# Kernel tuning notes

Hardware: AMD Instinct MI355X
Metric: run time of the kernel (lower is better)

## Reference

```python
import jax, jax.numpy as jnp
import numpy as np

NL = 8      # num layers (['self','cross']*4)
H = 8       # heads
EPS = 1e-5  # torch LayerNorm default


def _layernorm(x, g, b):
    mu = jnp.mean(x, axis=-1, keepdims=True)
    var = jnp.mean((x - mu) ** 2, axis=-1, keepdims=True)
    return (x - mu) * jax.lax.rsqrt(var + EPS) * g + b


def _encoder_layer(x, source, Wq, Wk, Wv, Wm, W1, W2, g1, b1, g2, b2):
    # x: [N, L, C], source: [N, S, C]
    N, L, C = x.shape
    D = C // H
    q = (x @ Wq).reshape(N, L, H, D)
    k = (source @ Wk).reshape(N, -1, H, D)
    v = (source @ Wv).reshape(N, -1, H, D)
    # naive full attention: explicit [N, L, S, H] scores (as in FullAttention)
    qk = jnp.einsum('nlhd,nshd->nlsh', q, k)
    A = jax.nn.softmax(qk * (1.0 / np.sqrt(D)), axis=2)
    msg = jnp.einsum('nlsh,nshd->nlhd', A, v).reshape(N, L, C)
    msg = _layernorm(msg @ Wm, g1, b1)
    m = jnp.concatenate([x, msg], axis=-1)          # [N, L, 2C]
    m = jax.nn.relu(m @ W1) @ W2                    # [N, L, C]
    m = _layernorm(m, g2, b2)
    return x + m


def _loftr(feat0, feat1, Wq, Wk, Wv, Wm, W1, W2, g1, b1, g2, b2):
    names = ['self', 'cross'] * 4
    for i, name in enumerate(names):
        p = (Wq[i], Wk[i], Wv[i], Wm[i], W1[i], W2[i], g1[i], b1[i], g2[i], b2[i])
        if name == 'self':
            feat0 = _encoder_layer(feat0, feat0, *p)
            feat1 = _encoder_layer(feat1, feat1, *p)
        else:  # cross; note feat0 is updated before being fed to feat1's layer
            feat0 = _encoder_layer(feat0, feat1, *p)
            feat1 = _encoder_layer(feat1, feat0, *p)
    return jnp.stack([feat0, feat1], axis=0)  # [2, N, L, C]


def setup_inputs() -> dict:
    key = jax.random.key(0)
    ks = jax.random.split(key, 10)
    N, L, C = 8, 1024, 768
    s = 1.0 / np.sqrt(C)       # xavier-ish scale for [C, C]
    s2 = 1.0 / np.sqrt(2 * C)  # for MLP fan-in 2C
    return {
        'feat0': jax.random.normal(ks[0], (N, L, C), jnp.float32),
        'feat1': jax.random.normal(ks[1], (N, L, C), jnp.float32),
        'Wq': jax.random.normal(ks[2], (NL, C, C), jnp.float32) * s,
        'Wk': jax.random.normal(ks[3], (NL, C, C), jnp.float32) * s,
        'Wv': jax.random.normal(ks[4], (NL, C, C), jnp.float32) * s,
        'Wm': jax.random.normal(ks[5], (NL, C, C), jnp.float32) * s,
        'W1': jax.random.normal(ks[6], (NL, 2 * C, 2 * C), jnp.float32) * s2,
        'W2': jax.random.normal(ks[7], (NL, 2 * C, C), jnp.float32) * s2,
        'g1': jnp.ones((NL, C), jnp.float32),
        'b1': jnp.zeros((NL, C), jnp.float32),
        'g2': jnp.ones((NL, C), jnp.float32),
        'b2': jnp.zeros((NL, C), jnp.float32),
    }


def reference(feat0, feat1, Wq, Wk, Wv, Wm, W1, W2, g1, b1, g2, b2):
    return _loftr(feat0, feat1, Wq, Wk, Wv, Wm, W1, W2, g1, b1, g2, b2)
```

## Files before the change

kernel.cpp:

```cpp
#include <hip/hip_runtime.h>
#include <hip/hip_bf16.h>

typedef __hip_bfloat16 bf16;
typedef __bf16 bf16x8 __attribute__((ext_vector_type(8)));
typedef float f32x4 __attribute__((ext_vector_type(4)));

#define AS1 __attribute__((address_space(1)))
#define AS3 __attribute__((address_space(3)))
__device__ __forceinline__ void gl_lds16(const void* g, void* l) {
    __builtin_amdgcn_global_load_lds((const AS1 void*)g, (AS3 void*)l, 16, 0, 0);
}

__device__ __forceinline__ float fexp2(float x) {
#if __has_builtin(__builtin_amdgcn_exp2f)
    return __builtin_amdgcn_exp2f(x);
#else
    return exp2f(x);
#endif
}

__device__ __forceinline__ int xcd_swz(int did, int nwg) {
    return (did & 7) * (nwg >> 3) + (did >> 3);
}


__global__ __launch_bounds__(256) void cvt_f32_bf16_k(const float* __restrict__ in, bf16* __restrict__ out,
                                                      int ostride, int total)
{
    int i = blockIdx.x * 256 + threadIdx.x;
    int e = i * 4;
    if (e >= total) return;
    int row = e / 768;
    int col = e - row * 768;
    const float4 f = *(const float4*)(in + e);
    bf16 o4[4];
    o4[0] = __float2bfloat16(f.x); o4[1] = __float2bfloat16(f.y);
    o4[2] = __float2bfloat16(f.z); o4[3] = __float2bfloat16(f.w);
    *(uint2*)(out + (size_t)row * ostride + col) = *(uint2*)o4;
}

__global__ void transpose_cvt_k(const float* __restrict__ in, bf16* __restrict__ out, int R, int C,
                                float scale, size_t lstride)
{
    __shared__ float t[32][33];
    const int tx = threadIdx.x, ty = threadIdx.y;
    in  += (size_t)blockIdx.z * R * C;
    out += (size_t)blockIdx.z * lstride;
    const int c0 = blockIdx.x * 32, r0 = blockIdx.y * 32;
    #pragma unroll
    for (int i = 0; i < 4; ++i)
        t[ty + i*8][tx] = in[(size_t)(r0 + ty + i*8) * C + c0 + tx];
    __syncthreads();
    #pragma unroll
    for (int i = 0; i < 4; ++i)
        out[(size_t)(c0 + ty + i*8) * R + r0 + tx] = __float2bfloat16(t[tx][ty + i*8] * scale);
}

template<int EPI>
__global__ __launch_bounds__(256) void gemm_bt_k(const bf16* __restrict__ A, int lda,
                                                 const bf16* __restrict__ BT, int K,
                                                 void* __restrict__ Cp, int ldc, int colshift,
                                                 bf16* __restrict__ Ck, bf16* __restrict__ Cv)
{
    __shared__ bf16 a_sm[3][4096];
    __shared__ bf16 b_sm[3][4096];
    const int tid = threadIdx.x;
    const int lane = tid & 63;
    const int wid = tid >> 6;
    const int wr = wid >> 1, wc = wid & 1;

    const int nwg = gridDim.x * gridDim.y;
    const int did = blockIdx.x + gridDim.x * blockIdx.y;
    const int wgid = xcd_swz(did, nwg);
    const int col0 = (wgid % gridDim.y) * 128;
    const int row0 = (wgid / gridDim.y) * 128;
    const int g = lane >> 4, r16 = lane & 15;

    const int r4 = lane >> 2;
    const int sc = (lane & 3) ^ ((lane >> 3) & 3);
    const bf16* gA[2]; const bf16* gB[2]; int loff[2];
    #pragma unroll
    for (int i = 0; i < 2; ++i) {
        const int blk = wid*2 + i;
        gA[i] = A  + (size_t)(row0 + blk*16 + r4) * lda + sc*8;
        gB[i] = BT + (size_t)(col0 + blk*16 + r4) * K   + sc*8;
        loff[i] = blk * 512;
    }
    const int foff = r16*32 + ((g ^ ((r16 >> 1) & 3)) * 8);

    f32x4 acc[4][4];
    #pragma unroll
    for (int m = 0; m < 4; ++m)
        #pragma unroll
        for (int n = 0; n < 4; ++n)
            #pragma unroll
            for (int r = 0; r < 4; ++r) acc[m][n][r] = 0.f;

    #pragma unroll
    for (int i = 0; i < 2; ++i) {
        gl_lds16(gA[i],      &a_sm[0][loff[i]]);
        gl_lds16(gB[i],      &b_sm[0][loff[i]]);
    }
    #pragma unroll
    for (int i = 0; i < 2; ++i) {
        gl_lds16(gA[i] + 32, &a_sm[1][loff[i]]);
        gl_lds16(gB[i] + 32, &b_sm[1][loff[i]]);
    }

    int cur = 0, pre = 2;
    for (int k0 = 0; k0 < K; k0 += 32) {
        if (k0 + 32 < K) asm volatile("s_waitcnt vmcnt(4)" ::: "memory");
        else             asm volatile("s_waitcnt vmcnt(0)" ::: "memory");
        __builtin_amdgcn_s_barrier();
        if (k0 + 64 < K) {
            #pragma unroll
            for (int i = 0; i < 2; ++i) {
                gl_lds16(gA[i] + k0 + 64, &a_sm[pre][loff[i]]);
                gl_lds16(gB[i] + k0 + 64, &b_sm[pre][loff[i]]);
            }
        }
        bf16x8 af[4], bfr[4];
        #pragma unroll
        for (int m = 0; m < 4; ++m) af[m]  = *(const bf16x8*)&a_sm[cur][(wr*4 + m)*512 + foff];
        #pragma unroll
        for (int n = 0; n < 4; ++n) bfr[n] = *(const bf16x8*)&b_sm[cur][(wc*4 + n)*512 + foff];
        asm volatile("s_waitcnt lgkmcnt(0)" ::: "memory");
        __builtin_amdgcn_s_setprio(1);
        #pragma unroll
        for (int m = 0; m < 4; ++m)
            #pragma unroll
            for (int n = 0; n < 4; ++n)
                acc[m][n] = __builtin_amdgcn_mfma_f32_16x16x32_bf16(af[m], bfr[n], acc[m][n], 0, 0, 0);
        __builtin_amdgcn_s_setprio(0);
        cur = (cur == 2) ? 0 : cur + 1;
        pre = (pre == 2) ? 0 : pre + 1;
    }

    #pragma unroll
    for (int m = 0; m < 4; ++m) {
        const int orow = row0 + wr*64 + m*16 + g*4;
        #pragma unroll
        for (int n = 0; n < 4; ++n) {
            const int ocol = col0 + wc*64 + n*16 + r16;
            if (EPI == 4 || EPI == 5) {
                const int ce = ocol + colshift;
                const int seg = ce / 768;
                const int ci = ce - seg*768;
                if (seg <= 1) {
                    bf16* dst = (seg == 0) ? (bf16*)Cp : Ck;
                    #pragma unroll
                    for (int r = 0; r < 4; ++r)
                        dst[(size_t)(orow + r)*768 + ci] = __float2bfloat16(acc[m][n][r]);
                } else {
                    const int nn = orow >> 10, ss = orow & 1023;
                    const int hh = ci / 96, dd = ci - hh * 96;
                    bf16 pk[4];
                    #pragma unroll
                    for (int r = 0; r < 4; ++r) pk[r] = __float2bfloat16(acc[m][n][r]);
                    *(uint2*)&Cv[(((size_t)nn*8 + hh)*96 + dd)*1024 + ss] = *(uint2*)pk;
                }
            } else {
                #pragma unroll
                for (int r = 0; r < 4; ++r) {
                    float v = acc[m][n][r];
                    if (EPI == 1) v = fmaxf(v, 0.f);
                    ((bf16*)Cp)[(size_t)(orow + r)*ldc + ocol] = __float2bfloat16(v);
                }
            }
        }
    }
}

__global__ __launch_bounds__(512) void attn_k(const bf16* __restrict__ qb, const bf16* __restrict__ kb,
                                              const bf16* __restrict__ vtb, bf16* __restrict__ msgb)
{
    __shared__ bf16 kv_sm[3][12*512];
    __shared__ bf16 p_sm_all[8][32][40];
    const int tid = threadIdx.x;
    const int lane = tid & 63;
    const int w = tid >> 6;
    const int g = lane >> 4, r16 = lane & 15;

    const int nwg = gridDim.x * gridDim.y;
    const int did = blockIdx.x + gridDim.x * blockIdx.y;
    const int wgid = xcd_swz(did, nwg);
    const int qx = wgid % gridDim.x;
    const int nh = wgid / gridDim.x;
    const int n = nh >> 3, h = nh & 7;
    const int q0 = qx * 256 + w * 32;

    bf16 (*p_sm)[40] = p_sm_all[w];

    const bf16* kbase = kb  + ((size_t)n*1024)*768 + (size_t)h*96;
    const bf16* vbase = vtb + ((size_t)(n*8 + h))*96*1024;

    bf16x8 aq[2][3];
    #pragma unroll
    for (int qh = 0; qh < 2; ++qh) {
        const size_t qoff = ((size_t)n*1024 + q0 + qh*16 + r16) * 768 + (size_t)h*96;
        #pragma unroll
        for (int c = 0; c < 3; ++c) aq[qh][c] = *(const bf16x8*)&qb[qoff + c*32 + g*8];
    }

    const int r4 = lane >> 2;
    const int sc = (lane & 3) ^ ((lane >> 3) & 3);
    const bf16* gsrc[2]; size_t gstep[2]; int dstoff[2];
    const int nissue = (w < 4) ? 2 : 1;
    #pragma unroll
    for (int jj = 0; jj < 2; ++jj) {
        const int issue = w + jj*8;
        if (issue < 6) {
            const int c = issue >> 1, kh = issue & 1;
            gsrc[jj]  = kbase + (size_t)(kh*16 + r4)*768 + c*32 + sc*8;
            gstep[jj] = 768;
        } else {
            gsrc[jj]  = vbase + (size_t)((issue-6)*16 + r4)*1024 + sc*8;
            gstep[jj] = 1;
        }
        dstoff[jj] = (issue < 12) ? issue * 512 : 0;
    }
    const int foff = r16*32 + ((g ^ ((r16 >> 1) & 3)) * 8);

    float m_run[2], l_run[2];
    #pragma unroll
    for (int qh = 0; qh < 2; ++qh) { m_run[qh] = -1e30f; l_run[qh] = 0.f; }
    f32x4 o[2][6];
    #pragma unroll
    for (int qg = 0; qg < 2; ++qg)
        #pragma unroll
        for (int f = 0; f < 6; ++f)
            #pragma unroll
            for (int r = 0; r < 4; ++r) o[qg][f][r] = 0.f;

    gl_lds16(gsrc[0], &kv_sm[0][dstoff[0]]);
    if (nissue == 2) gl_lds16(gsrc[1], &kv_sm[0][dstoff[1]]);
    gl_lds16(gsrc[0] + 32 * gstep[0], &kv_sm[1][dstoff[0]]);
    if (nissue == 2) gl_lds16(gsrc[1] + 32 * gstep[1], &kv_sm[1][dstoff[1]]);

    int cur = 0, pre = 2;
    for (int kt = 0; kt < 1024; kt += 32) {
        if (kt + 32 < 1024) {
            if (nissue == 2) asm volatile("s_waitcnt vmcnt(2)" ::: "memory");
            else             asm volatile("s_waitcnt vmcnt(1)" ::: "memory");
        } else {
            asm volatile("s_waitcnt vmcnt(0)" ::: "memory");
        }
        __builtin_amdgcn_s_barrier();
        if (kt + 64 < 1024) {
            gl_lds16(gsrc[0] + (size_t)(kt + 64) * gstep[0], &kv_sm[pre][dstoff[0]]);
            if (nissue == 2) gl_lds16(gsrc[1] + (size_t)(kt + 64) * gstep[1], &kv_sm[pre][dstoff[1]]);
        }
        const bf16* rd = kv_sm[cur];

        f32x4 s[2][2];
        #pragma unroll
        for (int kh = 0; kh < 2; ++kh)
            #pragma unroll
            for (int qh = 0; qh < 2; ++qh)
                #pragma unroll
                for (int r = 0; r < 4; ++r) s[kh][qh][r] = 0.f;
        __builtin_amdgcn_s_setprio(1);
        #pragma unroll
        for (int c = 0; c < 3; ++c) {
            bf16x8 ak0 = *(const bf16x8*)&rd[(c*2 + 0)*512 + foff];
            bf16x8 ak1 = *(const bf16x8*)&rd[(c*2 + 1)*512 + foff];
            s[0][0] = __builtin_amdgcn_mfma_f32_16x16x32_bf16(ak0, aq[0][c], s[0][0], 0, 0, 0);
            s[0][1] = __builtin_amdgcn_mfma_f32_16x16x32_bf16(ak0, aq[1][c], s[0][1], 0, 0, 0);
            s[1][0] = __builtin_amdgcn_mfma_f32_16x16x32_bf16(ak1, aq[0][c], s[1][0], 0, 0, 0);
            s[1][1] = __builtin_amdgcn_mfma_f32_16x16x32_bf16(ak1, aq[1][c], s[1][1], 0, 0, 0);
        }
        __builtin_amdgcn_s_setprio(0);

        float pmv[2], gr[2];
        #pragma unroll
        for (int qh = 0; qh < 2; ++qh) {
            float pm = fmaxf(fmaxf(fmaxf(s[0][qh][0], s[0][qh][1]), fmaxf(s[0][qh][2], s[0][qh][3])),
                             fmaxf(fmaxf(s[1][qh][0], s[1][qh][1]), fmaxf(s[1][qh][2], s[1][qh][3])));
            pm = fmaxf(pm, __shfl_xor(pm, 16, 64));
            pm = fmaxf(pm, __shfl_xor(pm, 32, 64));
            pmv[qh] = pm;
            gr[qh] = pm - m_run[qh];
        }
        if (__any(fmaxf(gr[0], gr[1]) > 8.0f)) {
            float alpha_c[2];
            #pragma unroll
            for (int qh = 0; qh < 2; ++qh) {
                float mn = fmaxf(m_run[qh], pmv[qh]);
                alpha_c[qh] = fexp2(m_run[qh] - mn);
                m_run[qh] = mn;
                l_run[qh] *= alpha_c[qh];
            }
            #pragma unroll
            for (int qg = 0; qg < 2; ++qg)
                #pragma unroll
                for (int r = 0; r < 4; ++r) {
                    float ar = __shfl(alpha_c[qg], g*4 + r, 64);
                    #pragma unroll
                    for (int f = 0; f < 6; ++f) o[qg][f][r] *= ar;
                }
        }
        #pragma unroll
        for (int qh = 0; qh < 2; ++qh) {
            bf16 pk0[4], pk1[4];
            float rs = 0.f;
            #pragma unroll
            for (int r = 0; r < 4; ++r) {
                float p0 = fexp2(s[0][qh][r] - m_run[qh]);
                float p1 = fexp2(s[1][qh][r] - m_run[qh]);
                rs += p0 + p1;
                pk0[r] = __float2bfloat16(p0);
                pk1[r] = __float2bfloat16(p1);
            }
            rs += __shfl_xor(rs, 16, 64);
            rs += __shfl_xor(rs, 32, 64);
            l_run[qh] += rs;
            *(uint2*)&p_sm[qh*16 + r16][g*4]      = *(uint2*)pk0;
            *(uint2*)&p_sm[qh*16 + r16][16 + g*4] = *(uint2*)pk1;
        }

        bf16x8 pa0 = *(const bf16x8*)&p_sm[r16][g*8];
        bf16x8 pa1 = *(const bf16x8*)&p_sm[16 + r16][g*8];
        __builtin_amdgcn_s_setprio(1);
        #pragma unroll
        for (int f = 0; f < 6; ++f) {
            bf16x8 bv = *(const bf16x8*)&rd[(6 + f)*512 + foff];
            o[0][f] = __builtin_amdgcn_mfma_f32_16x16x32_bf16(pa0, bv, o[0][f], 0, 0, 0);
            o[1][f] = __builtin_amdgcn_mfma_f32_16x16x32_bf16(pa1, bv, o[1][f], 0, 0, 0);
        }
        __builtin_amdgcn_s_setprio(0);
        asm volatile("s_waitcnt lgkmcnt(0)" ::: "memory");
        cur = (cur == 2) ? 0 : cur + 1;
        pre = (pre == 2) ? 0 : pre + 1;
    }

    float linv[2][4];
    #pragma unroll
    for (int qg = 0; qg < 2; ++qg)
        #pragma unroll
        for (int r = 0; r < 4; ++r)
            linv[qg][r] = 1.0f / __shfl(l_run[qg], g*4 + r, 64);

    #pragma unroll
    for (int qg = 0; qg < 2; ++qg) {
        const size_t obase = ((size_t)n*1024 + q0 + qg*16 + g*4) * 768 + (size_t)h*96;
        #pragma unroll
        for (int f = 0; f < 6; ++f)
            #pragma unroll
            for (int r = 0; r < 4; ++r)
                msgb[obase + (size_t)r*768 + f*16 + r16] = __float2bfloat16(o[qg][f][r] * linv[qg][r]);
    }
}

template<int MODE>
__global__ __launch_bounds__(256) void ln_k(const bf16* __restrict__ in, const float* __restrict__ g,
                                            const float* __restrict__ b, bf16* __restrict__ outc,
                                            float* __restrict__ x)
{
    const int row = blockIdx.x;
    const int tid = threadIdx.x;
    const bf16* rp = in + (size_t)row * 768;
    float v[3];
    #pragma unroll
    for (int j = 0; j < 3; ++j) v[j] = __bfloat162float(rp[tid + j*256]);
    float s  = v[0] + v[1] + v[2];
    float sq = v[0]*v[0] + v[1]*v[1] + v[2]*v[2];
    #pragma unroll
    for (int off = 32; off >= 1; off >>= 1) {
        s  += __shfl_xor(s,  off, 64);
        sq += __shfl_xor(sq, off, 64);
    }
    __shared__ float red[2][4];
    const int wid = tid >> 6;
    if ((tid & 63) == 0) { red[0][wid] = s; red[1][wid] = sq; }
    __syncthreads();
    const float S  = red[0][0] + red[0][1] + red[0][2] + red[0][3];
    const float SQ = red[1][0] + red[1][1] + red[1][2] + red[1][3];
    const float mu = S * (1.f/768.f);
    float var = SQ * (1.f/768.f) - mu*mu;
    var = fmaxf(var, 0.f);
    const float rs = rsqrtf(var + 1e-5f);
    #pragma unroll
    for (int j = 0; j < 3; ++j) {
        const int c = tid + j*256;
        const float y = (v[j] - mu) * rs * g[c] + b[c];
        if (MODE == 1) {
            outc[(size_t)row*1536 + 768 + c] = __float2bfloat16(y);
        } else {
            const float nx = x[(size_t)row*768 + c] + y;
            x[(size_t)row*768 + c] = nx;
            outc[(size_t)row*1536 + c] = __float2bfloat16(nx);
        }
    }
}

extern "C" void kernel_launch(void* const* d_in, const int* in_sizes, int n_in,
                              void* d_out, int out_size, void* d_ws, size_t ws_size,
                              hipStream_t stream)
{
    const float* feat0 = (const float*)d_in[0];
    const float* feat1 = (const float*)d_in[1];
    const float* Wq = (const float*)d_in[2];
    const float* Wk = (const float*)d_in[3];
    const float* Wv = (const float*)d_in[4];
    const float* Wm = (const float*)d_in[5];
    const float* W1 = (const float*)d_in[6];
    const float* W2 = (const float*)d_in[7];
    const float* g1 = (const float*)d_in[8];
    const float* b1 = (const float*)d_in[9];
    const float* g2 = (const float*)d_in[10];
    const float* b2 = (const float*)d_in[11];

    bf16 *wqkvT, *wmT, *w1T, *w2T, *concat0, *concat1, *qb, *kb, *vtb, *m1b, *t0b;
    auto plan = [&](int RB) -> size_t {
        char* p = (char*)d_ws;
        auto take = [&](size_t bytes) { char* q = p; p += (bytes + 255) & ~(size_t)255; return q; };
        wqkvT = (bf16*)take((size_t)8*2304*768*2);
        wmT  = (bf16*)take((size_t)8*768*768*2);
        w1T  = (bf16*)take((size_t)8*1536*1536*2);
        w2T  = (bf16*)take((size_t)8*768*1536*2);
        concat0 = (bf16*)take((size_t)8192*1536*2);
        concat1 = (bf16*)take((size_t)8192*1536*2);
        qb   = (bf16*)take((size_t)RB*768*2);
        kb   = (bf16*)take((size_t)RB*768*2);
        vtb  = (bf16*)take((size_t)RB*768*2);
        m1b  = (bf16*)take((size_t)RB*1536*2);
        t0b  = (bf16*)take((size_t)RB*768*2);
        return (size_t)(p - (char*)d_ws);
    };
    bool batched = plan(16384) <= ws_size;
    if (!batched) plan(8192);
    bf16* msgb = qb;

    float* x0 = (float*)d_out;
    float* x1 = x0 + (size_t)8192*768;

    hipMemcpyAsync(x0, feat0, (size_t)8192*768*4, hipMemcpyDeviceToDevice, stream);
    hipMemcpyAsync(x1, feat1, (size_t)8192*768*4, hipMemcpyDeviceToDevice, stream);

    const float s_qk = 0.14724444f;
    const dim3 tb(32, 8);
    const size_t QKV = (size_t)2304*768;
    transpose_cvt_k<<<dim3(24,24,8), tb, 0, stream>>>(Wq, wqkvT,            768, 768,  s_qk, QKV);
    transpose_cvt_k<<<dim3(24,24,8), tb, 0, stream>>>(Wk, wqkvT + 768*768,  768, 768,  1.0f, QKV);
    transpose_cvt_k<<<dim3(24,24,8), tb, 0, stream>>>(Wv, wqkvT + 1536*768, 768, 768,  1.0f, QKV);
    transpose_cvt_k<<<dim3(24,24,8), tb, 0, stream>>>(Wm, wmT, 768, 768,  1.0f, (size_t)768*768);
    transpose_cvt_k<<<dim3(48,48,8), tb, 0, stream>>>(W1, w1T, 1536, 1536, 1.0f, (size_t)1536*1536);
    transpose_cvt_k<<<dim3(24,48,8), tb, 0, stream>>>(W2, w2T, 1536, 768,  1.0f, (size_t)1536*768);

    const int total = 8192*768;
    cvt_f32_bf16_k<<<6144, 256, 0, stream>>>(feat0, concat0, 1536, total);
    cvt_f32_bf16_k<<<6144, 256, 0, stream>>>(feat1, concat1, 1536, total);

    auto encode = [&](float* x, bf16* cS, const bf16* cR, int i, bool self, int M) {
        const bf16* wl = wqkvT + (size_t)i * QKV;
        const int MT = M / 128;
        if (self) {
            gemm_bt_k<4><<<dim3(MT,18), 256, 0, stream>>>(cS, 1536, wl, 768, qb, 768, 0, kb, vtb);
        } else {
            gemm_bt_k<0><<<dim3(MT,6),  256, 0, stream>>>(cS, 1536, wl, 768, qb, 768, 0, nullptr, nullptr);
            gemm_bt_k<5><<<dim3(MT,12), 256, 0, stream>>>(cR, 1536, wl + (size_t)768*768, 768,
                                                          nullptr, 0, 768, kb, vtb);
        }
        attn_k<<<dim3(4, (M/1024)*8), 512, 0, stream>>>(qb, kb, vtb, msgb);
        gemm_bt_k<0><<<dim3(MT,6),  256, 0, stream>>>(msgb, 768, wmT + (size_t)i*768*768, 768,
                                                      t0b, 768, 0, nullptr, nullptr);
        ln_k<1><<<M, 256, 0, stream>>>(t0b, g1 + i*768, b1 + i*768, cS, nullptr);
        gemm_bt_k<1><<<dim3(MT,12), 256, 0, stream>>>(cS, 1536, w1T + (size_t)i*1536*1536, 1536,
                                                      m1b, 1536, 0, nullptr, nullptr);
        gemm_bt_k<0><<<dim3(MT,6),  256, 0, stream>>>(m1b, 1536, w2T + (size_t)i*768*1536, 1536,
                                                      t0b, 768, 0, nullptr, nullptr);
        ln_k<2><<<M, 256, 0, stream>>>(t0b, g2 + i*768, b2 + i*768, cS, x);
    };

    for (int i = 0; i < 8; ++i) {
        if ((i & 1) == 0) {
            if (batched) {
                encode(x0, concat0, concat0, i, true, 16384);
            } else {
                encode(x0, concat0, concat0, i, true, 8192);
                encode(x1, concat1, concat1, i, true, 8192);
            }
        } else {
            encode(x0, concat0, concat1, i, false, 8192);
            encode(x1, concat1, concat0, i, false, 8192);
        }
    }
}
```

Before: 3.440 ms.

## Software-pipeline LDS fragment loads with register double-buffering in GEMM main loop

```diff
diff --git a/kernel.cpp b/kernel.cpp
--- a/kernel.cpp
+++ b/kernel.cpp
@@ -106,35 +106,69 @@
         gl_lds16(gA[i] + 32, &a_sm[1][loff[i]]);
         gl_lds16(gB[i] + 32, &b_sm[1][loff[i]]);
     }
-
-    int cur = 0, pre = 2;
-    for (int k0 = 0; k0 < K; k0 += 32) {
-        if (k0 + 32 < K) asm volatile("s_waitcnt vmcnt(4)" ::: "memory");
-        else             asm volatile("s_waitcnt vmcnt(0)" ::: "memory");
-        __builtin_amdgcn_s_barrier();
-        if (k0 + 64 < K) {
-            #pragma unroll
-            for (int i = 0; i < 2; ++i) {
-                gl_lds16(gA[i] + k0 + 64, &a_sm[pre][loff[i]]);
-                gl_lds16(gB[i] + k0 + 64, &b_sm[pre][loff[i]]);
-            }
-        }
-        bf16x8 af[4], bfr[4];
-        #pragma unroll
-        for (int m = 0; m < 4; ++m) af[m]  = *(const bf16x8*)&a_sm[cur][(wr*4 + m)*512 + foff];
-        #pragma unroll
-        for (int n = 0; n < 4; ++n) bfr[n] = *(const bf16x8*)&b_sm[cur][(wc*4 + n)*512 + foff];
-        asm volatile("s_waitcnt lgkmcnt(0)" ::: "memory");
+    asm volatile("s_waitcnt vmcnt(0)" ::: "memory");
+    __builtin_amdgcn_s_barrier();
+
+    bf16x8 afX[4], bfX[4], afY[4], bfY[4];
+    #pragma unroll
+    for (int m = 0; m < 4; ++m) afX[m] = *(const bf16x8*)&a_sm[0][(wr*4 + m)*512 + foff];
+    #pragma unroll
+    for (int n = 0; n < 4; ++n) bfX[n] = *(const bf16x8*)&b_sm[0][(wc*4 + n)*512 + foff];
+
+    int s1 = 1, s2 = 2;
+    const int NT = K >> 5;
+
+#define HALF_ITER(T, afT, bfT, afN, bfN, DO_STAGE)                                          \
+    {                                                                                       \
+        _Pragma("unroll")                                                                   \
+        for (int m = 0; m < 4; ++m) afN[m] = *(const bf16x8*)&a_sm[s1][(wr*4 + m)*512 + foff]; \
+        _Pragma("unroll")                                                                   \
+        for (int n = 0; n < 4; ++n) bfN[n] = *(const bf16x8*)&b_sm[s1][(wc*4 + n)*512 + foff]; \
+        if (DO_STAGE) {                                                                     \
+            _Pragma("unroll")                                                               \
+            for (int i = 0; i < 2; ++i) {                                                   \
+                gl_lds16(gA[i] + (T)*32 + 64, &a_sm[s2][loff[i]]);                          \
+                gl_lds16(gB[i] + (T)*32 + 64, &b_sm[s2][loff[i]]);                          \
+            }                                                                               \
+        }                                                                                   \
+        __builtin_amdgcn_sched_barrier(0);           \
+        __builtin_amdgcn_s_setprio(1);                                                      \
+        _Pragma("unroll")                                                                   \
+        for (int m = 0; m < 4; ++m)                                                         \
+            _Pragma("unroll")                                                               \
+            for (int n = 0; n < 4; ++n)                                                     \
+                acc[m][n] = __builtin_amdgcn_mfma_f32_16x16x32_bf16(afT[m], bfT[n], acc[m][n], 0, 0, 0); \
+        __builtin_amdgcn_s_setprio(0);                                                      \
+        asm volatile("s_waitcnt vmcnt(0)" ::: "memory");             \
+        __builtin_amdgcn_s_barrier();                                                       \
+        s1 = (s1 == 2) ? 0 : s1 + 1;                                                        \
+        s2 = (s2 == 2) ? 0 : s2 + 1;                                                        \
+    }
+
+    for (int t = 0; t < NT - 2; t += 2) {
+        HALF_ITER(t,     afX, bfX, afY, bfY, true);
+        HALF_ITER(t + 1, afY, bfY, afX, bfX, true);
+    }
+    {
+        #pragma unroll
+        for (int m = 0; m < 4; ++m) afY[m] = *(const bf16x8*)&a_sm[s1][(wr*4 + m)*512 + foff];
+        #pragma unroll
+        for (int n = 0; n < 4; ++n) bfY[n] = *(const bf16x8*)&b_sm[s1][(wc*4 + n)*512 + foff];
+        __builtin_amdgcn_sched_barrier(0);
         __builtin_amdgcn_s_setprio(1);
         #pragma unroll
         for (int m = 0; m < 4; ++m)
             #pragma unroll
             for (int n = 0; n < 4; ++n)
-                acc[m][n] = __builtin_amdgcn_mfma_f32_16x16x32_bf16(af[m], bfr[n], acc[m][n], 0, 0, 0);
+                acc[m][n] = __builtin_amdgcn_mfma_f32_16x16x32_bf16(afX[m], bfX[n], acc[m][n], 0, 0, 0);
+        #pragma unroll
+        for (int m = 0; m < 4; ++m)
+            #pragma unroll
+            for (int n = 0; n < 4; ++n)
+                acc[m][n] = __builtin_amdgcn_mfma_f32_16x16x32_bf16(afY[m], bfY[n], acc[m][n], 0, 0, 0);
         __builtin_amdgcn_s_setprio(0);
-        cur = (cur == 2) ? 0 : cur + 1;
-        pre = (pre == 2) ? 0 : pre + 1;
-    }
+    }
+#undef HALF_ITER
 
     #pragma unroll
     for (int m = 0; m < 4; ++m) {
```

Result: slower. 3.526 ms (+2.5%).

## Give each attention wave 64 query rows using 4-wave blocks

Applied to the files above, without the earlier changes.

```diff
diff --git a/kernel.cpp b/kernel.cpp
--- a/kernel.cpp
+++ b/kernel.cpp
@@ -171,11 +171,11 @@
     }
 }
 
-__global__ __launch_bounds__(512) void attn_k(const bf16* __restrict__ qb, const bf16* __restrict__ kb,
+__global__ __launch_bounds__(256) void attn_k(const bf16* __restrict__ qb, const bf16* __restrict__ kb,
                                               const bf16* __restrict__ vtb, bf16* __restrict__ msgb)
 {
     __shared__ bf16 kv_sm[3][12*512];
-    __shared__ bf16 p_sm_all[8][32][40];
+    __shared__ bf16 p_sm_all[4][64][40];
     const int tid = threadIdx.x;
     const int lane = tid & 63;
     const int w = tid >> 6;
@@ -187,16 +187,16 @@
     const int qx = wgid % gridDim.x;
     const int nh = wgid / gridDim.x;
     const int n = nh >> 3, h = nh & 7;
-    const int q0 = qx * 256 + w * 32;
+    const int q0 = qx * 256 + w * 64;
 
     bf16 (*p_sm)[40] = p_sm_all[w];
 
     const bf16* kbase = kb  + ((size_t)n*1024)*768 + (size_t)h*96;
     const bf16* vbase = vtb + ((size_t)(n*8 + h))*96*1024;
 
-    bf16x8 aq[2][3];
-    #pragma unroll
-    for (int qh = 0; qh < 2; ++qh) {
+    bf16x8 aq[4][3];
+    #pragma unroll
+    for (int qh = 0; qh < 4; ++qh) {
         const size_t qoff = ((size_t)n*1024 + q0 + qh*16 + r16) * 768 + (size_t)h*96;
         #pragma unroll
         for (int c = 0; c < 3; ++c) aq[qh][c] = *(const bf16x8*)&qb[qoff + c*32 + g*8];
@@ -204,11 +204,10 @@
 
     const int r4 = lane >> 2;
     const int sc = (lane & 3) ^ ((lane >> 3) & 3);
-    const bf16* gsrc[2]; size_t gstep[2]; int dstoff[2];
-    const int nissue = (w < 4) ? 2 : 1;
-    #pragma unroll
-    for (int jj = 0; jj < 2; ++jj) {
-        const int issue = w + jj*8;
+    const bf16* gsrc[3]; size_t gstep[3]; int dstoff[3];
+    #pragma unroll
+    for (int jj = 0; jj < 3; ++jj) {
+        const int issue = w + jj*4;
         if (issue < 6) {
             const int c = issue >> 1, kh = issue & 1;
             gsrc[jj]  = kbase + (size_t)(kh*16 + r4)*768 + c*32 + sc*8;
@@ -217,46 +216,43 @@
             gsrc[jj]  = vbase + (size_t)((issue-6)*16 + r4)*1024 + sc*8;
             gstep[jj] = 1;
         }
-        dstoff[jj] = (issue < 12) ? issue * 512 : 0;
+        dstoff[jj] = issue * 512;
     }
     const int foff = r16*32 + ((g ^ ((r16 >> 1) & 3)) * 8);
 
-    float m_run[2], l_run[2];
-    #pragma unroll
-    for (int qh = 0; qh < 2; ++qh) { m_run[qh] = -1e30f; l_run[qh] = 0.f; }
-    f32x4 o[2][6];
-    #pragma unroll
-    for (int qg = 0; qg < 2; ++qg)
+    float m_run[4], l_run[4];
+    #pragma unroll
+    for (int qh = 0; qh < 4; ++qh) { m_run[qh] = -1e30f; l_run[qh] = 0.f; }
+    f32x4 o[4][6];
+    #pragma unroll
+    for (int qg = 0; qg < 4; ++qg)
         #pragma unroll
         for (int f = 0; f < 6; ++f)
             #pragma unroll
             for (int r = 0; r < 4; ++r) o[qg][f][r] = 0.f;
 
-    gl_lds16(gsrc[0], &kv_sm[0][dstoff[0]]);
-    if (nissue == 2) gl_lds16(gsrc[1], &kv_sm[0][dstoff[1]]);
-    gl_lds16(gsrc[0] + 32 * gstep[0], &kv_sm[1][dstoff[0]]);
-    if (nissue == 2) gl_lds16(gsrc[1] + 32 * gstep[1], &kv_sm[1][dstoff[1]]);
+    #pragma unroll
+    for (int jj = 0; jj < 3; ++jj) gl_lds16(gsrc[jj], &kv_sm[0][dstoff[jj]]);
+    #pragma unroll
+    for (int jj = 0; jj < 3; ++jj) gl_lds16(gsrc[jj] + 32 * gstep[jj], &kv_sm[1][dstoff[jj]]);
 
     int cur = 0, pre = 2;
     for (int kt = 0; kt < 1024; kt += 32) {
-        if (kt + 32 < 1024) {
-            if (nissue == 2) asm volatile("s_waitcnt vmcnt(2)" ::: "memory");
-            else             asm volatile("s_waitcnt vmcnt(1)" ::: "memory");
-        } else {
-            asm volatile("s_waitcnt vmcnt(0)" ::: "memory");
-        }
+        if (kt + 32 < 1024) asm volatile("s_waitcnt vmcnt(3)" ::: "memory");
+        else                asm volatile("s_waitcnt vmcnt(0)" ::: "memory");
         __builtin_amdgcn_s_barrier();
         if (kt + 64 < 1024) {
-            gl_lds16(gsrc[0] + (size_t)(kt + 64) * gstep[0], &kv_sm[pre][dstoff[0]]);
-            if (nissue == 2) gl_lds16(gsrc[1] + (size_t)(kt + 64) * gstep[1], &kv_sm[pre][dstoff[1]]);
+            #pragma unroll
+            for (int jj = 0; jj < 3; ++jj)
+                gl_lds16(gsrc[jj] + (size_t)(kt + 64) * gstep[jj], &kv_sm[pre][dstoff[jj]]);
         }
         const bf16* rd = kv_sm[cur];
 
-        f32x4 s[2][2];
+        f32x4 s[2][4];
         #pragma unroll
         for (int kh = 0; kh < 2; ++kh)
             #pragma unroll
-            for (int qh = 0; qh < 2; ++qh)
+            for (int qh = 0; qh < 4; ++qh)
                 #pragma unroll
                 for (int r = 0; r < 4; ++r) s[kh][qh][r] = 0.f;
         __builtin_amdgcn_s_setprio(1);
@@ -264,16 +260,17 @@
         for (int c = 0; c < 3; ++c) {
             bf16x8 ak0 = *(const bf16x8*)&rd[(c*2 + 0)*512 + foff];
             bf16x8 ak1 = *(const bf16x8*)&rd[(c*2 + 1)*512 + foff];
-            s[0][0] = __builtin_amdgcn_mfma_f32_16x16x32_bf16(ak0, aq[0][c], s[0][0], 0, 0, 0);
-            s[0][1] = __builtin_amdgcn_mfma_f32_16x16x32_bf16(ak0, aq[1][c], s[0][1], 0, 0, 0);
-            s[1][0] = __builtin_amdgcn_mfma_f32_16x16x32_bf16(ak1, aq[0][c], s[1][0], 0, 0, 0);
-            s[1][1] = __builtin_amdgcn_mfma_f32_16x16x32_bf16(ak1, aq[1][c], s[1][1], 0, 0, 0);
+            #pragma unroll
+            for (int qh = 0; qh < 4; ++qh) {
+                s[0][qh] = __builtin_amdgcn_mfma_f32_16x16x32_bf16(ak0, aq[qh][c], s[0][qh], 0, 0, 0);
+                s[1][qh] = __builtin_amdgcn_mfma_f32_16x16x32_bf16(ak1, aq[qh][c], s[1][qh], 0, 0, 0);
+            }
         }
         __builtin_amdgcn_s_setprio(0);
 
-        float pmv[2], gr[2];
-        #pragma unroll
-        for (int qh = 0; qh < 2; ++qh) {
+        float pmv[4], gr[4];
+        #pragma unroll
+        for (int qh = 0; qh < 4; ++qh) {
             float pm = fmaxf(fmaxf(fmaxf(s[0][qh][0], s[0][qh][1]), fmaxf(s[0][qh][2], s[0][qh][3])),
                              fmaxf(fmaxf(s[1][qh][0], s[1][qh][1]), fmaxf(s[1][qh][2], s[1][qh][3])));
             pm = fmaxf(pm, __shfl_xor(pm, 16, 64));
@@ -281,17 +278,18 @@
             pmv[qh] = pm;
             gr[qh] = pm - m_run[qh];
         }
-        if (__any(fmaxf(gr[0], gr[1]) > 8.0f)) {
-            float alpha_c[2];
-            #pragma unroll
-            for (int qh = 0; qh < 2; ++qh) {
+        const float grmax = fmaxf(fmaxf(gr[0], gr[1]), fmaxf(gr[2], gr[3]));
+        if (__any(grmax > 8.0f)) {
+            float alpha_c[4];
+            #pragma unroll
+            for (int qh = 0; qh < 4; ++qh) {
                 float mn = fmaxf(m_run[qh], pmv[qh]);
                 alpha_c[qh] = fexp2(m_run[qh] - mn);
                 m_run[qh] = mn;
                 l_run[qh] *= alpha_c[qh];
             }
             #pragma unroll
-            for (int qg = 0; qg < 2; ++qg)
+            for (int qg = 0; qg < 4; ++qg)
                 #pragma unroll
                 for (int r = 0; r < 4; ++r) {
                     float ar = __shfl(alpha_c[qg], g*4 + r, 64);
@@ -300,7 +298,7 @@
                 }
         }
         #pragma unroll
-        for (int qh = 0; qh < 2; ++qh) {
+        for (int qh = 0; qh < 4; ++qh) {
             bf16 pk0[4], pk1[4];
             float rs = 0.f;
             #pragma unroll
@@ -318,14 +316,18 @@
             *(uint2*)&p_sm[qh*16 + r16][16 + g*4] = *(uint2*)pk1;
         }
 
-        bf16x8 pa0 = *(const bf16x8*)&p_sm[r16][g*8];
+        bf16x8 pa0 = *(const bf16x8*)&p_sm[     r16][g*8];
         bf16x8 pa1 = *(const bf16x8*)&p_sm[16 + r16][g*8];
+        bf16x8 pa2 = *(const bf16x8*)&p_sm[32 + r16][g*8];
+        bf16x8 pa3 = *(const bf16x8*)&p_sm[48 + r16][g*8];
         __builtin_amdgcn_s_setprio(1);
         #pragma unroll
         for (int f = 0; f < 6; ++f) {
             bf16x8 bv = *(const bf16x8*)&rd[(6 + f)*512 + foff];
             o[0][f] = __builtin_amdgcn_mfma_f32_16x16x32_bf16(pa0, bv, o[0][f], 0, 0, 0);
             o[1][f] = __builtin_amdgcn_mfma_f32_16x16x32_bf16(pa1, bv, o[1][f], 0, 0, 0);
+            o[2][f] = __builtin_amdgcn_mfma_f32_16x16x32_bf16(pa2, bv, o[2][f], 0, 0, 0);
+            o[3][f] = __builtin_amdgcn_mfma_f32_16x16x32_bf16(pa3, bv, o[3][f], 0, 0, 0);
         }
         __builtin_amdgcn_s_setprio(0);
         asm volatile("s_waitcnt lgkmcnt(0)" ::: "memory");
@@ -333,15 +335,15 @@
         pre = (pre == 2) ? 0 : pre + 1;
     }
 
-    float linv[2][4];
-    #pragma unroll
-    for (int qg = 0; qg < 2; ++qg)
+    float linv[4][4];
+    #pragma unroll
+    for (int qg = 0; qg < 4; ++qg)
         #pragma unroll
         for (int r = 0; r < 4; ++r)
             linv[qg][r] = 1.0f / __shfl(l_run[qg], g*4 + r, 64);
 
     #pragma unroll
-    for (int qg = 0; qg < 2; ++qg) {
+    for (int qg = 0; qg < 4; ++qg) {
         const size_t obase = ((size_t)n*1024 + q0 + qg*16 + g*4) * 768 + (size_t)h*96;
         #pragma unroll
         for (int f = 0; f < 6; ++f)
@@ -461,7 +463,7 @@
             gemm_bt_k<5><<<dim3(MT,12), 256, 0, stream>>>(cR, 1536, wl + (size_t)768*768, 768,
                                                           nullptr, 0, 768, kb, vtb);
         }
-        attn_k<<<dim3(4, (M/1024)*8), 512, 0, stream>>>(qb, kb, vtb, msgb);
+        attn_k<<<dim3(4, (M/1024)*8), 256, 0, stream>>>(qb, kb, vtb, msgb);
         gemm_bt_k<0><<<dim3(MT,6),  256, 0, stream>>>(msgb, 768, wmT + (size_t)i*768*768, 768,
                                                       t0b, 768, 0, nullptr, nullptr);
         ln_k<1><<<M, 256, 0, stream>>>(t0b, g1 + i*768, b1 + i*768, cS, nullptr);
```

Result: slower. 3.823 ms (+11.1%).
